# Kernel optimization log

Hardware: AMD Instinct MI355X
Metric: run time of the kernel (lower is better)

## Reference

```python
import jax, jax.numpy as jnp
import numpy as np

BINS = 10


def _neg_pearson(p, t):
    # global standardization (torch.std default is unbiased, ddof=1)
    p = (p - p.mean()) / p.std(ddof=1)
    t = (t - t.mean()) / t.std(ddof=1)
    N = p.shape[1]
    sx = p.sum(1); sy = t.sum(1)
    sxy = (p * t).sum(1)
    sx2 = (p * p).sum(1); sy2 = (t * t).sum(1)
    pear = (N * sxy - sx * sy) / jnp.sqrt((N * sx2 - sx**2) * (N * sy2 - sy**2))
    return (1.0 - pear).mean()


def _hann(N):
    # torch.hann_window is periodic: 0.5*(1 - cos(2*pi*n/N))
    return 0.5 * (1.0 - jnp.cos(2.0 * jnp.pi * jnp.arange(N, dtype=jnp.float32) / N))


def _phase_correlation(x, t):
    # torch.stft with n_fft=seq_len, center=False, hann window -> single frame = rfft(x*hann)
    N = x.shape[1]
    w = _hann(N)
    xf = jnp.fft.rfft(x * w, axis=1)   # [B, N//2+1]
    tf = jnp.fft.rfft(t * w, axis=1)
    corr = xf * jnp.conj(tf)
    corr = corr / jnp.abs(corr)        # phase-only correlation
    cm = jnp.fft.irfft(corr, n=N, axis=1)  # [B, N]
    idx = jnp.argmax(cm, axis=1)
    return 1.0 - jnp.mean(jnp.cos(2.0 * jnp.pi * idx / N))


def _power_spectrum(x, t):
    xp = jnp.abs(jnp.fft.rfft(x, axis=1)) ** 2
    tp = jnp.abs(jnp.fft.rfft(t, axis=1)) ** 2
    return jnp.mean(jnp.abs(xp - tp)) / jnp.mean(tp)


def _mutual_information(x, y, bins=BINS):
    B, S = x.shape
    xmin = x.min(1); xmax = x.max(1)
    ymin = y.min(1); ymax = y.max(1)
    bwx = (xmax - xmin) / bins
    bwy = (ymax - ymin) / bins
    ix = jnp.clip(((x - xmin[:, None]) / bwx[:, None]).astype(jnp.int32), 0, bins - 1)
    iy = jnp.clip(((y - ymin[:, None]) / bwy[:, None]).astype(jnp.int32), 0, bins - 1)
    flat = ix * bins + iy  # [B, S]
    # vectorized 2D histogram via scatter-add (replaces the python double loop)
    hist = jax.vmap(lambda f: jnp.zeros(bins * bins, jnp.float32).at[f].add(1.0))(flat)
    hist = hist.reshape(B, bins, bins)
    hx = hist.sum(2); hy = hist.sum(1)
    denom = B * S  # NOTE: original normalizes by batch*seq (faithful reproduction)
    px = hx / denom; py = hy / denom; pxy = hist / denom
    eps = 1e-8
    mi = (pxy * jnp.log((pxy + eps) / (px[:, :, None] * py[:, None, :] + eps))).sum((1, 2))
    hxe = -(px * jnp.log(px + eps)).sum(1)
    hye = -(py * jnp.log(py + eps)).sum(1)
    nmi = mi / ((hxe + hye) / 2.0)
    return 1.0 - nmi.mean()


def setup_inputs() -> dict:
    key = jax.random.key(0)
    k1, k2 = jax.random.split(key)
    return {
        "predictions": jax.random.normal(k1, (2, 512, 16384), dtype=jnp.float32),
        "targets": jax.random.normal(k2, (512, 16384), dtype=jnp.float32),
        "i": 0,
        "epoch": 700,
    }


def reference(predictions, targets, i, epoch):
    p = predictions[i]  # [B, S]
    loss = _neg_pearson(p, targets)
    if epoch >= 400:
        loss = loss + _phase_correlation(p, targets)
        loss = loss + _power_spectrum(p, targets)
    if epoch >= 700:
        loss = loss + _mutual_information(p, targets)
    return loss
```

## Files before the change

### kernel.cpp

```cpp
#include <hip/hip_runtime.h>
#include <math.h>

#define BB 512
#define SS 16384
#define TPIF 6.28318530717958647692f

#define PAD32(i) ((i) + ((i) >> 5) + ((i) >> 10))
#define NPAD 16912

__device__ __forceinline__ int digrev4(int n) {
    unsigned x = __brev((unsigned)n) >> (32 - 14);
    return (int)(((x & 0x1555u) << 1) | ((x >> 1) & 0x1555u));
}


template <int SGN, int LOG2Q>
__device__ __forceinline__ void stage_dif4(float* sre, float* sim, int t) {
    constexpr int Q = 1 << LOG2Q;
    const float sg = (float)SGN;
    #pragma unroll 2
    for (int c = 0; c < 4; ++c) {
        const int j = 4 * t + c;
        const int g = j >> LOG2Q;
        const int p = j & (Q - 1);
        const int e0 = (g << (LOG2Q + 2)) + p;
        const int i0 = PAD32(e0);
        const int i1 = PAD32(e0 + Q);
        const int i2 = PAD32(e0 + 2 * Q);
        const int i3 = PAD32(e0 + 3 * Q);
        float z0r = sre[i0], z0i = sim[i0];
        float z1r = sre[i1], z1i = sim[i1];
        float z2r = sre[i2], z2i = sim[i2];
        float z3r = sre[i3], z3i = sim[i3];
        float t0r = z0r + z2r, t0i = z0i + z2i;
        float t1r = z0r - z2r, t1i = z0i - z2i;
        float t2r = z1r + z3r, t2i = z1i + z3i;
        float t3r = z1r - z3r, t3i = z1i - z3i;
        float b0r = t0r + t2r, b0i = t0i + t2i;
        float b2r = t0r - t2r, b2i = t0i - t2i;
        float b1r = t1r - sg * t3i, b1i = t1i + sg * t3r;
        float b3r = t1r + sg * t3i, b3i = t1i - sg * t3r;
        const float a = sg * (float)p * (1.0f / (4.0f * (float)Q));
        const float cb = __builtin_amdgcn_cosf(a);
        const float sb = __builtin_amdgcn_sinf(a);
        const float w2r = cb * cb - sb * sb, w2i = 2.0f * cb * sb;
        const float w3r = cb * w2r - sb * w2i, w3i = cb * w2i + sb * w2r;
        sre[i0] = b0r;                    sim[i0] = b0i;
        sre[i1] = b1r * cb - b1i * sb;    sim[i1] = b1r * sb + b1i * cb;
        sre[i2] = b2r * w2r - b2i * w2i;  sim[i2] = b2r * w2i + b2i * w2r;
        sre[i3] = b3r * w3r - b3i * w3i;  sim[i3] = b3r * w3i + b3i * w3r;
    }
    __syncthreads();
}

template <int SGN, int LOG2Q>
__device__ __forceinline__ void stage_dit4(float* sre, float* sim, int t) {
    constexpr int Q = 1 << LOG2Q;
    const float sg = (float)SGN;
    #pragma unroll 2
    for (int c = 0; c < 4; ++c) {
        const int j = 4 * t + c;
        const int g = j >> LOG2Q;
        const int p = j & (Q - 1);
        const int e0 = (g << (LOG2Q + 2)) + p;
        const int i0 = PAD32(e0);
        const int i1 = PAD32(e0 + Q);
        const int i2 = PAD32(e0 + 2 * Q);
        const int i3 = PAD32(e0 + 3 * Q);
        float z0r = sre[i0], z0i = sim[i0];
        float z1r = sre[i1], z1i = sim[i1];
        float z2r = sre[i2], z2i = sim[i2];
        float z3r = sre[i3], z3i = sim[i3];
        const float a = sg * (float)p * (1.0f / (4.0f * (float)Q));
        const float cb = __builtin_amdgcn_cosf(a);
        const float sb = __builtin_amdgcn_sinf(a);
        const float w2r = cb * cb - sb * sb, w2i = 2.0f * cb * sb;
        const float w3r = cb * w2r - sb * w2i, w3i = cb * w2i + sb * w2r;
        float a1r = z1r * cb - z1i * sb,   a1i = z1r * sb + z1i * cb;
        float a2r = z2r * w2r - z2i * w2i, a2i = z2r * w2i + z2i * w2r;
        float a3r = z3r * w3r - z3i * w3i, a3i = z3r * w3i + z3i * w3r;
        float t0r = z0r + a2r, t0i = z0i + a2i;
        float t1r = z0r - a2r, t1i = z0i - a2i;
        float t2r = a1r + a3r, t2i = a1i + a3i;
        float t3r = a1r - a3r, t3i = a1i - a3i;
        sre[i0] = t0r + t2r;       sim[i0] = t0i + t2i;
        sre[i2] = t0r - t2r;       sim[i2] = t0i - t2i;
        sre[i1] = t1r - sg * t3i;  sim[i1] = t1i + sg * t3r;
        sre[i3] = t1r + sg * t3i;  sim[i3] = t1i - sg * t3r;
    }
    __syncthreads();
}

__global__ __launch_bounds__(1024, 4) void k_main(const float* __restrict__ pred,
                                                  const float* __restrict__ targ,
                                                  const int* __restrict__ ip,
                                                  float* __restrict__ wpear,
                                                  float* __restrict__ wcos,
                                                  double* __restrict__ wnum,
                                                  double* __restrict__ wden,
                                                  float* __restrict__ wnmi) {
    __shared__ float sre[NPAD];
    __shared__ float sim[NPAD];
    __shared__ double dpart[16 * 5];
    __shared__ float fpart[16 * 4];
    __shared__ int   subhist[400];
    __shared__ float hxm[10], hym[10];
    __shared__ float mterm[128];
    __shared__ float sbounds[4];
    __shared__ float svalw[16];
    __shared__ int   sidxw[16];

    const int row = blockIdx.x;
    const int t = threadIdx.x;
    const int w = t >> 6;
    const int lane = t & 63;

    const float* xg = pred + (size_t)ip[0] * (size_t)BB * SS + (size_t)row * SS;
    const float* yg = targ + (size_t)row * SS;

    {
        const float4* xg4 = reinterpret_cast<const float4*>(xg);
        const float4* yg4 = reinterpret_cast<const float4*>(yg);
        double sx = 0, sy = 0, sxy = 0, sxx = 0, syy = 0;
        float xmn = 3.4e38f, xmx = -3.4e38f, ymn = 3.4e38f, ymx = -3.4e38f;
        #pragma unroll
        for (int m2 = 0; m2 < 4; ++m2) {
            int idx = t + (m2 << 10);
            float4 a = xg4[idx];
            float4 b = yg4[idx];
            int n0 = idx << 2;
            sre[PAD32(n0 + 0)] = a.x; sim[PAD32(n0 + 0)] = b.x;
            sre[PAD32(n0 + 1)] = a.y; sim[PAD32(n0 + 1)] = b.y;
            sre[PAD32(n0 + 2)] = a.z; sim[PAD32(n0 + 2)] = b.z;
            sre[PAD32(n0 + 3)] = a.w; sim[PAD32(n0 + 3)] = b.w;
            float av[4] = {a.x, a.y, a.z, a.w};
            float bv[4] = {b.x, b.y, b.z, b.w};
            #pragma unroll
            for (int c = 0; c < 4; ++c) {
                float aa = av[c], bb = bv[c];
                sx += (double)aa; sy += (double)bb;
                sxy += (double)aa * (double)bb;
                sxx += (double)aa * (double)aa;
                syy += (double)bb * (double)bb;
                xmn = fminf(xmn, aa); xmx = fmaxf(xmx, aa);
                ymn = fminf(ymn, bb); ymx = fmaxf(ymx, bb);
            }
        }
        #pragma unroll
        for (int o = 32; o > 0; o >>= 1) {
            sx += __shfl_down(sx, o, 64);  sy += __shfl_down(sy, o, 64);
            sxy += __shfl_down(sxy, o, 64);
            sxx += __shfl_down(sxx, o, 64); syy += __shfl_down(syy, o, 64);
            xmn = fminf(xmn, __shfl_down(xmn, o, 64));
            xmx = fmaxf(xmx, __shfl_down(xmx, o, 64));
            ymn = fminf(ymn, __shfl_down(ymn, o, 64));
            ymx = fmaxf(ymx, __shfl_down(ymx, o, 64));
        }
        if (lane == 0) {
            dpart[w*5+0] = sx; dpart[w*5+1] = sy; dpart[w*5+2] = sxy;
            dpart[w*5+3] = sxx; dpart[w*5+4] = syy;
            fpart[w*4+0] = xmn; fpart[w*4+1] = xmx; fpart[w*4+2] = ymn; fpart[w*4+3] = ymx;
        }
    }
    if (t < 400) subhist[t] = 0;
    __syncthreads();
    if (t == 0) {
        double v0=0,v1=0,v2=0,v3=0,v4=0;
        float b0=fpart[0], b1=fpart[1], b2=fpart[2], b3=fpart[3];
        for (int q = 0; q < 16; ++q) {
            v0 += dpart[q*5]; v1 += dpart[q*5+1]; v2 += dpart[q*5+2];
            v3 += dpart[q*5+3]; v4 += dpart[q*5+4];
            b0 = fminf(b0, fpart[q*4]);   b1 = fmaxf(b1, fpart[q*4+1]);
            b2 = fminf(b2, fpart[q*4+2]); b3 = fmaxf(b3, fpart[q*4+3]);
        }
        double N = (double)SS;
        double num = N * v2 - v0 * v1;
        double den = sqrt((N * v3 - v0 * v0) * (N * v4 - v1 * v1));
        wpear[row] = (float)(1.0 - num / den);
        sbounds[0] = b0; sbounds[1] = b1; sbounds[2] = b2; sbounds[3] = b3;
    }
    __syncthreads();

    {
        const float x0 = sbounds[0], bwx = (sbounds[1] - x0) / 10.0f;
        const float y0 = sbounds[2], bwy = (sbounds[3] - y0) / 10.0f;
        int* hsub = subhist + ((t >> 6) & 3) * 100;
        #pragma unroll 2
        for (int m = 0; m < 16; ++m) {
            int ii = PAD32(t + (m << 10));
            float a = sre[ii], b = sim[ii];
            int ix = (int)((a - x0) / bwx); ix = min(max(ix, 0), 9);
            int iy = (int)((b - y0) / bwy); iy = min(max(iy, 0), 9);
            atomicAdd(&hsub[ix * 10 + iy], 1);
        }
    }
    __syncthreads();
    if (t < 100) subhist[t] = subhist[t] + subhist[100+t] + subhist[200+t] + subhist[300+t];
    __syncthreads();
    if (t < 10) {
        int s1 = 0, s2 = 0;
        for (int j = 0; j < 10; ++j) { s1 += subhist[t*10+j]; s2 += subhist[j*10+t]; }
        hxm[t] = (float)s1; hym[t] = (float)s2;
    }
    __syncthreads();
    {
        float term = 0.0f;
        if (t < 100) {
            const float denom = 8388608.0f, eps = 1e-8f;
            float pxy = (float)subhist[t] / denom;
            float px = hxm[t / 10] / denom, py = hym[t % 10] / denom;
            term = pxy * logf((pxy + eps) / (px * py + eps));
        }
        if (t < 128) mterm[t] = (t < 100) ? term : 0.0f;
    }
    __syncthreads();
    if (t == 0) {
        const float denom = 8388608.0f, eps = 1e-8f;
        float mi = 0.0f;
        for (int q = 0; q < 100; ++q) mi += mterm[q];
        float hxe = 0.0f, hye = 0.0f;
        for (int q = 0; q < 10; ++q) {
            float px = hxm[q] / denom, py = hym[q] / denom;
            hxe -= px * logf(px + eps);
            hye -= py * logf(py + eps);
        }
        wnmi[row] = mi / (0.5f * (hxe + hye));
    }
    __syncthreads();

    stage_dif4<-1, 12>(sre, sim, t);
    stage_dif4<-1, 10>(sre, sim, t);
    stage_dif4<-1,  8>(sre, sim, t);
    stage_dif4<-1,  6>(sre, sim, t);
    stage_dif4<-1,  4>(sre, sim, t);
    stage_dif4<-1,  2>(sre, sim, t);
    stage_dif4<-1,  0>(sre, sim, t);

    {
        double anum = 0.0, aden = 0.0;
        float crv[8], civ[8];
        #pragma unroll 1
        for (int m = 0; m < 8; ++m) {
            int k = t + (m << 10);
            int km = (SS - k) & (SS - 1);
            int qa = digrev4(k), qb = digrev4(km);
            float ar  = sre[PAD32(qa)], ai  = sim[PAD32(qa)];
            float cr0 = sre[PAD32(qb)], ci0 = sim[PAD32(qb)];
            float xr = 0.5f * (ar + cr0), xi = 0.5f * (ai - ci0);
            float yr = 0.5f * (ai + ci0), yi = 0.5f * (cr0 - ar);
            float xp = xr * xr + xi * xi;
            float tp = yr * yr + yi * yi;
            anum += (double)fabsf(xp - tp);
            aden += (double)tp;
            int qap = digrev4((k + 1) & (SS - 1));
            int qam = digrev4((k - 1) & (SS - 1));
            int qbp = digrev4((km + 1) & (SS - 1));
            int qbm = digrev4((km - 1) & (SS - 1));
            float apr = sre[PAD32(qap)], api = sim[PAD32(qap)];
            float amr = sre[PAD32(qam)], ami = sim[PAD32(qam)];
            float bpr = sre[PAD32(qbp)], bpi = sim[PAD32(qbp)];
            float bmr = sre[PAD32(qbm)], bmi = sim[PAD32(qbm)];
            float zwr = 0.5f * ar  - 0.25f * (apr + amr);
            float zwi = 0.5f * ai  - 0.25f * (api + ami);
            float vwr = 0.5f * cr0 - 0.25f * (bpr + bmr);
            float vwi = 0.5f * ci0 - 0.25f * (bpi + bmi);
            float xwr = 0.5f * (zwr + vwr), xwi = 0.5f * (zwi - vwi);
            float ywr = 0.5f * (zwi + vwi), ywi = 0.5f * (vwr - zwr);
            float cr = xwr * ywr + xwi * ywi;
            float ci = xwi * ywr - xwr * ywi;
            float mag = sqrtf(cr * cr + ci * ci);
            crv[m] = cr / mag; civ[m] = ci / mag;
        }
        float c8 = 0.0f;
        if (t == 0) {
            int q  = digrev4(8192);
            int qp = digrev4(8193);
            int qm = digrev4(8191);
            float ar = sre[PAD32(q)],  ai = sim[PAD32(q)];
            anum += (double)fabsf(ar * ar - ai * ai);
            aden += (double)(ai * ai);
            float zwr = 0.5f * ar - 0.25f * (sre[PAD32(qp)] + sre[PAD32(qm)]);
            float zwi = 0.5f * ai - 0.25f * (sim[PAD32(qp)] + sim[PAD32(qm)]);
            float pr = zwr * zwi;
            c8 = pr / fabsf(pr);
        }
        #pragma unroll
        for (int o = 32; o > 0; o >>= 1) {
            anum += __shfl_down(anum, o, 64);
            aden += __shfl_down(aden, o, 64);
        }
        if (lane == 0) { dpart[w*2] = anum; dpart[w*2+1] = aden; }
        __syncthreads();
        #pragma unroll
        for (int m = 0; m < 8; ++m) {
            int k = t + (m << 10);
            int km = (SS - k) & (SS - 1);
            int q = digrev4(k), q2 = digrev4(km);
            sre[PAD32(q)]  = crv[m]; sim[PAD32(q)]  = civ[m];
            sre[PAD32(q2)] = crv[m]; sim[PAD32(q2)] = -civ[m];
        }
        if (t == 0) {
            int q = digrev4(8192);
            sre[PAD32(q)] = c8; sim[PAD32(q)] = 0.0f;
            double a = 0, b = 0;
            for (int q2_ = 0; q2_ < 16; ++q2_) { a += dpart[q2_*2]; b += dpart[q2_*2+1]; }
            wnum[row] = a; wden[row] = b;
        }
    }
    __syncthreads();

    stage_dit4<1,  0>(sre, sim, t);
    stage_dit4<1,  2>(sre, sim, t);
    stage_dit4<1,  4>(sre, sim, t);
    stage_dit4<1,  6>(sre, sim, t);
    stage_dit4<1,  8>(sre, sim, t);
    stage_dit4<1, 10>(sre, sim, t);
    stage_dit4<1, 12>(sre, sim, t);

    {
        float bv = -3.4e38f; int bi = 0;
        #pragma unroll
        for (int m = 0; m < 16; ++m) {
            int n = t + (m << 10);
            float v = sre[PAD32(n)];
            if (v > bv) { bv = v; bi = n; }
        }
        #pragma unroll
        for (int o = 32; o > 0; o >>= 1) {
            float v2 = __shfl_down(bv, o, 64);
            int i2 = __shfl_down(bi, o, 64);
            if (v2 > bv || (v2 == bv && i2 < bi)) { bv = v2; bi = i2; }
        }
        if (lane == 0) { svalw[w] = bv; sidxw[w] = bi; }
    }
    __syncthreads();
    if (t == 0) {
        float bv = svalw[0]; int bi = sidxw[0];
        for (int q = 1; q < 16; ++q) {
            if (svalw[q] > bv || (svalw[q] == bv && sidxw[q] < bi)) { bv = svalw[q]; bi = sidxw[q]; }
        }
        wcos[row] = cosf(TPIF * (float)bi / 16384.0f);
    }
}

__global__ __launch_bounds__(512) void k_combine(const float* __restrict__ wpear,
                                                 const float* __restrict__ wcos,
                                                 const double* __restrict__ wnum,
                                                 const double* __restrict__ wden,
                                                 const float* __restrict__ wnmi,
                                                 const int* __restrict__ ep,
                                                 float* __restrict__ out) {
    __shared__ double dp[8 * 5];
    const int tid = threadIdx.x;
    const int w = tid >> 6, lane = tid & 63;
    double v0 = (double)wpear[tid], v1 = (double)wcos[tid];
    double v2 = wnum[tid], v3 = wden[tid], v4 = (double)wnmi[tid];
    #pragma unroll
    for (int o = 32; o > 0; o >>= 1) {
        v0 += __shfl_down(v0, o, 64); v1 += __shfl_down(v1, o, 64);
        v2 += __shfl_down(v2, o, 64); v3 += __shfl_down(v3, o, 64);
        v4 += __shfl_down(v4, o, 64);
    }
    if (lane == 0) {
        dp[w*5+0] = v0; dp[w*5+1] = v1; dp[w*5+2] = v2; dp[w*5+3] = v3; dp[w*5+4] = v4;
    }
    __syncthreads();
    if (tid == 0) {
        double s0=0,s1=0,s2=0,s3=0,s4=0;
        for (int q = 0; q < 8; ++q) {
            s0 += dp[q*5]; s1 += dp[q*5+1]; s2 += dp[q*5+2]; s3 += dp[q*5+3]; s4 += dp[q*5+4];
        }
        int epoch = ep[0];
        double loss = s0 / 512.0;
        if (epoch >= 400) {
            loss += 1.0 - s1 / 512.0;
            loss += s2 / s3;
        }
        if (epoch >= 700) {
            loss += 1.0 - s4 / 512.0;
        }
        out[0] = (float)loss;
    }
}

extern "C" void kernel_launch(void* const* d_in, const int* in_sizes, int n_in,
                              void* d_out, int out_size, void* d_ws, size_t ws_size,
                              hipStream_t stream) {
    const float* pred = (const float*)d_in[0];
    const float* targ = (const float*)d_in[1];
    const int* ip = (const int*)d_in[2];
    const int* ep = (const int*)d_in[3];
    float* out = (float*)d_out;

    double* wnum = (double*)d_ws;
    double* wden = wnum + BB;
    float* wpear = (float*)(wden + BB);
    float* wcos = wpear + BB;
    float* wnmi = wcos + BB;

    k_main<<<dim3(BB), dim3(1024), 0, stream>>>(pred, targ, ip, wpear, wcos, wnum, wden, wnmi);
    k_combine<<<dim3(1), dim3(512), 0, stream>>>(wpear, wcos, wnum, wden, wnmi, ep, out);
}
```

Before: 214.7 us.

## Interleave FFT real/imag in float2 shared array and remap butterfly thread indexing

Replaces the separate real and imaginary shared-memory arrays with one interleaved float2 array, so each complex element is read and written with a single 64-bit LDS access. The padding function changes to suit 8-byte elements. The butterfly-to-thread mapping becomes strided (t + c*1024) instead of contiguous, which changes which LDS addresses a wavefront touches together. The goal is fewer LDS instructions and fewer bank conflicts in the FFT stages. The trade-off is a larger padded footprint (about 140KB of LDS), and some stages may now see different conflict patterns.

Measured after the change: 208.3 us. 3.0% less time.

```diff
diff --git a/kernel.cpp b/kernel.cpp
--- a/kernel.cpp
+++ b/kernel.cpp
@@ -5,8 +5,8 @@
 #define SS 16384
 #define TPIF 6.28318530717958647692f
 
-#define PAD32(i) ((i) + ((i) >> 5) + ((i) >> 10))
-#define NPAD 16912
+#define PD(i) ((i) + ((i) >> 4) + ((i) >> 8))
+#define NPD 17472
 
 __device__ __forceinline__ int digrev4(int n) {
     unsigned x = __brev((unsigned)n) >> (32 - 14);
@@ -15,27 +15,24 @@
 
 
 template <int SGN, int LOG2Q>
-__device__ __forceinline__ void stage_dif4(float* sre, float* sim, int t) {
+__device__ __forceinline__ void stage_dif4(float2* sz, int t) {
     constexpr int Q = 1 << LOG2Q;
     const float sg = (float)SGN;
     #pragma unroll 2
     for (int c = 0; c < 4; ++c) {
-        const int j = 4 * t + c;
+        const int j = t + (c << 10);
         const int g = j >> LOG2Q;
         const int p = j & (Q - 1);
         const int e0 = (g << (LOG2Q + 2)) + p;
-        const int i0 = PAD32(e0);
-        const int i1 = PAD32(e0 + Q);
-        const int i2 = PAD32(e0 + 2 * Q);
-        const int i3 = PAD32(e0 + 3 * Q);
-        float z0r = sre[i0], z0i = sim[i0];
-        float z1r = sre[i1], z1i = sim[i1];
-        float z2r = sre[i2], z2i = sim[i2];
-        float z3r = sre[i3], z3i = sim[i3];
-        float t0r = z0r + z2r, t0i = z0i + z2i;
-        float t1r = z0r - z2r, t1i = z0i - z2i;
-        float t2r = z1r + z3r, t2i = z1i + z3i;
-        float t3r = z1r - z3r, t3i = z1i - z3i;
+        const int i0 = PD(e0);
+        const int i1 = PD(e0 + Q);
+        const int i2 = PD(e0 + 2 * Q);
+        const int i3 = PD(e0 + 3 * Q);
+        float2 z0 = sz[i0], z1 = sz[i1], z2 = sz[i2], z3 = sz[i3];
+        float t0r = z0.x + z2.x, t0i = z0.y + z2.y;
+        float t1r = z0.x - z2.x, t1i = z0.y - z2.y;
+        float t2r = z1.x + z3.x, t2i = z1.y + z3.y;
+        float t3r = z1.x - z3.x, t3i = z1.y - z3.y;
         float b0r = t0r + t2r, b0i = t0i + t2i;
         float b2r = t0r - t2r, b2i = t0i - t2i;
         float b1r = t1r - sg * t3i, b1i = t1i + sg * t3r;
@@ -45,48 +42,45 @@
         const float sb = __builtin_amdgcn_sinf(a);
         const float w2r = cb * cb - sb * sb, w2i = 2.0f * cb * sb;
         const float w3r = cb * w2r - sb * w2i, w3i = cb * w2i + sb * w2r;
-        sre[i0] = b0r;                    sim[i0] = b0i;
-        sre[i1] = b1r * cb - b1i * sb;    sim[i1] = b1r * sb + b1i * cb;
-        sre[i2] = b2r * w2r - b2i * w2i;  sim[i2] = b2r * w2i + b2i * w2r;
-        sre[i3] = b3r * w3r - b3i * w3i;  sim[i3] = b3r * w3i + b3i * w3r;
+        sz[i0] = make_float2(b0r, b0i);
+        sz[i1] = make_float2(b1r * cb - b1i * sb,   b1r * sb + b1i * cb);
+        sz[i2] = make_float2(b2r * w2r - b2i * w2i, b2r * w2i + b2i * w2r);
+        sz[i3] = make_float2(b3r * w3r - b3i * w3i, b3r * w3i + b3i * w3r);
     }
     __syncthreads();
 }
 
 template <int SGN, int LOG2Q>
-__device__ __forceinline__ void stage_dit4(float* sre, float* sim, int t) {
+__device__ __forceinline__ void stage_dit4(float2* sz, int t) {
     constexpr int Q = 1 << LOG2Q;
     const float sg = (float)SGN;
     #pragma unroll 2
     for (int c = 0; c < 4; ++c) {
-        const int j = 4 * t + c;
+        const int j = t + (c << 10);
         const int g = j >> LOG2Q;
         const int p = j & (Q - 1);
         const int e0 = (g << (LOG2Q + 2)) + p;
-        const int i0 = PAD32(e0);
-        const int i1 = PAD32(e0 + Q);
-        const int i2 = PAD32(e0 + 2 * Q);
-        const int i3 = PAD32(e0 + 3 * Q);
-        float z0r = sre[i0], z0i = sim[i0];
-        float z1r = sre[i1], z1i = sim[i1];
-        float z2r = sre[i2], z2i = sim[i2];
-        float z3r = sre[i3], z3i = sim[i3];
+        const int i0 = PD(e0);
+        const int i1 = PD(e0 + Q);
+        const int i2 = PD(e0 + 2 * Q);
+        const int i3 = PD(e0 + 3 * Q);
+        float2 z0 = sz[i0], z1 = sz[i1], z2 = sz[i2], z3 = sz[i3];
         const float a = sg * (float)p * (1.0f / (4.0f * (float)Q));
         const float cb = __builtin_amdgcn_cosf(a);
         const float sb = __builtin_amdgcn_sinf(a);
         const float w2r = cb * cb - sb * sb, w2i = 2.0f * cb * sb;
         const float w3r = cb * w2r - sb * w2i, w3i = cb * w2i + sb * w2r;
-        float a1r = z1r * cb - z1i * sb,   a1i = z1r * sb + z1i * cb;
-        float a2r = z2r * w2r - z2i * w2i, a2i = z2r * w2i + z2i * w2r;
-        float a3r = z3r * w3r - z3i * w3i, a3i = z3r * w3i + z3i * w3r;
-        float t0r = z0r + a2r, t0i = z0i + a2i;
-        float t1r = z0r - a2r, t1i = z0i - a2i;
+        float a1r = z1.x * cb - z1.y * sb,   a1i = z1.x * sb + z1.y * cb;
+        float a2r = z2.x * w2r - z2.y * w2i, a2i = z2.x * w2i + z2.y * w2r;
+        float a3r = z3.x * w3r - z3.y * w3i, a3i = z3.x * w3i + z3.y * w3r;
+        float t0r = z0.x + a2r, t0i = z0.y + a2i;
+        float t1r = z0.x - a2r, t1i = z0.y - a2i;
         float t2r = a1r + a3r, t2i = a1i + a3i;
         float t3r = a1r - a3r, t3i = a1i - a3i;
-        sre[i0] = t0r + t2r;       sim[i0] = t0i + t2i;
-        sre[i2] = t0r - t2r;       sim[i2] = t0i - t2i;
-        sre[i1] = t1r - sg * t3i;  sim[i1] = t1i + sg * t3r;
-        sre[i3] = t1r + sg * t3i;  sim[i3] = t1i - sg * t3r;
+        sz[i0] = make_float2(t0r + t2r, t0i + t2i);
+        sz[i2] = make_float2(t0r - t2r, t0i - t2i);
+        sz[i1] = make_float2(t1r - sg * t3i, t1i + sg * t3r);
+        sz[i3] = make_float2(t1r + sg * t3i, t1i - sg * t3r);
     }
     __syncthreads();
 }
@@ -99,8 +93,7 @@
                                                   double* __restrict__ wnum,
                                                   double* __restrict__ wden,
                                                   float* __restrict__ wnmi) {
-    __shared__ float sre[NPAD];
-    __shared__ float sim[NPAD];
+    __shared__ float2 sz[NPD];
     __shared__ double dpart[16 * 5];
     __shared__ float fpart[16 * 4];
     __shared__ int   subhist[400];
@@ -129,10 +122,10 @@
             float4 a = xg4[idx];
             float4 b = yg4[idx];
             int n0 = idx << 2;
-            sre[PAD32(n0 + 0)] = a.x; sim[PAD32(n0 + 0)] = b.x;
-            sre[PAD32(n0 + 1)] = a.y; sim[PAD32(n0 + 1)] = b.y;
-            sre[PAD32(n0 + 2)] = a.z; sim[PAD32(n0 + 2)] = b.z;
-            sre[PAD32(n0 + 3)] = a.w; sim[PAD32(n0 + 3)] = b.w;
+            sz[PD(n0 + 0)] = make_float2(a.x, b.x);
+            sz[PD(n0 + 1)] = make_float2(a.y, b.y);
+            sz[PD(n0 + 2)] = make_float2(a.z, b.z);
+            sz[PD(n0 + 3)] = make_float2(a.w, b.w);
             float av[4] = {a.x, a.y, a.z, a.w};
             float bv[4] = {b.x, b.y, b.z, b.w};
             #pragma unroll
@@ -187,10 +180,9 @@
         int* hsub = subhist + ((t >> 6) & 3) * 100;
         #pragma unroll 2
         for (int m = 0; m < 16; ++m) {
-            int ii = PAD32(t + (m << 10));
-            float a = sre[ii], b = sim[ii];
-            int ix = (int)((a - x0) / bwx); ix = min(max(ix, 0), 9);
-            int iy = (int)((b - y0) / bwy); iy = min(max(iy, 0), 9);
+            float2 v = sz[PD(t + (m << 10))];
+            int ix = (int)((v.x - x0) / bwx); ix = min(max(ix, 0), 9);
+            int iy = (int)((v.y - y0) / bwy); iy = min(max(iy, 0), 9);
             atomicAdd(&hsub[ix * 10 + iy], 1);
         }
     }
@@ -228,13 +220,13 @@
     }
     __syncthreads();
 
-    stage_dif4<-1, 12>(sre, sim, t);
-    stage_dif4<-1, 10>(sre, sim, t);
-    stage_dif4<-1,  8>(sre, sim, t);
-    stage_dif4<-1,  6>(sre, sim, t);
-    stage_dif4<-1,  4>(sre, sim, t);
-    stage_dif4<-1,  2>(sre, sim, t);
-    stage_dif4<-1,  0>(sre, sim, t);
+    stage_dif4<-1, 12>(sz, t);
+    stage_dif4<-1, 10>(sz, t);
+    stage_dif4<-1,  8>(sz, t);
+    stage_dif4<-1,  6>(sz, t);
+    stage_dif4<-1,  4>(sz, t);
+    stage_dif4<-1,  2>(sz, t);
+    stage_dif4<-1,  0>(sz, t);
 
     {
         double anum = 0.0, aden = 0.0;
@@ -244,26 +236,24 @@
             int k = t + (m << 10);
             int km = (SS - k) & (SS - 1);
             int qa = digrev4(k), qb = digrev4(km);
-            float ar  = sre[PAD32(qa)], ai  = sim[PAD32(qa)];
-            float cr0 = sre[PAD32(qb)], ci0 = sim[PAD32(qb)];
+            float2 za = sz[PD(qa)];
+            float2 zb = sz[PD(qb)];
+            float ar  = za.x, ai  = za.y;
+            float cr0 = zb.x, ci0 = zb.y;
             float xr = 0.5f * (ar + cr0), xi = 0.5f * (ai - ci0);
             float yr = 0.5f * (ai + ci0), yi = 0.5f * (cr0 - ar);
             float xp = xr * xr + xi * xi;
             float tp = yr * yr + yi * yi;
             anum += (double)fabsf(xp - tp);
             aden += (double)tp;
-            int qap = digrev4((k + 1) & (SS - 1));
-            int qam = digrev4((k - 1) & (SS - 1));
-            int qbp = digrev4((km + 1) & (SS - 1));
-            int qbm = digrev4((km - 1) & (SS - 1));
-            float apr = sre[PAD32(qap)], api = sim[PAD32(qap)];
-            float amr = sre[PAD32(qam)], ami = sim[PAD32(qam)];
-            float bpr = sre[PAD32(qbp)], bpi = sim[PAD32(qbp)];
-            float bmr = sre[PAD32(qbm)], bmi = sim[PAD32(qbm)];
-            float zwr = 0.5f * ar  - 0.25f * (apr + amr);
-            float zwi = 0.5f * ai  - 0.25f * (api + ami);
-            float vwr = 0.5f * cr0 - 0.25f * (bpr + bmr);
-            float vwi = 0.5f * ci0 - 0.25f * (bpi + bmi);
+            float2 zap = sz[PD(digrev4((k + 1) & (SS - 1)))];
+            float2 zam = sz[PD(digrev4((k - 1) & (SS - 1)))];
+            float2 zbp = sz[PD(digrev4((km + 1) & (SS - 1)))];
+            float2 zbm = sz[PD(digrev4((km - 1) & (SS - 1)))];
+            float zwr = 0.5f * ar  - 0.25f * (zap.x + zam.x);
+            float zwi = 0.5f * ai  - 0.25f * (zap.y + zam.y);
+            float vwr = 0.5f * cr0 - 0.25f * (zbp.x + zbm.x);
+            float vwi = 0.5f * ci0 - 0.25f * (zbp.y + zbm.y);
             float xwr = 0.5f * (zwr + vwr), xwi = 0.5f * (zwi - vwi);
             float ywr = 0.5f * (zwi + vwi), ywi = 0.5f * (vwr - zwr);
             float cr = xwr * ywr + xwi * ywi;
@@ -273,14 +263,14 @@
         }
         float c8 = 0.0f;
         if (t == 0) {
-            int q  = digrev4(8192);
-            int qp = digrev4(8193);
-            int qm = digrev4(8191);
-            float ar = sre[PAD32(q)],  ai = sim[PAD32(q)];
+            float2 z0 = sz[PD(digrev4(8192))];
+            float2 zp = sz[PD(digrev4(8193))];
+            float2 zm = sz[PD(digrev4(8191))];
+            float ar = z0.x, ai = z0.y;
             anum += (double)fabsf(ar * ar - ai * ai);
             aden += (double)(ai * ai);
-            float zwr = 0.5f * ar - 0.25f * (sre[PAD32(qp)] + sre[PAD32(qm)]);
-            float zwi = 0.5f * ai - 0.25f * (sim[PAD32(qp)] + sim[PAD32(qm)]);
+            float zwr = 0.5f * ar - 0.25f * (zp.x + zm.x);
+            float zwi = 0.5f * ai - 0.25f * (zp.y + zm.y);
             float pr = zwr * zwi;
             c8 = pr / fabsf(pr);
         }
@@ -296,12 +286,11 @@
             int k = t + (m << 10);
             int km = (SS - k) & (SS - 1);
             int q = digrev4(k), q2 = digrev4(km);
-            sre[PAD32(q)]  = crv[m]; sim[PAD32(q)]  = civ[m];
-            sre[PAD32(q2)] = crv[m]; sim[PAD32(q2)] = -civ[m];
+            sz[PD(q)]  = make_float2(crv[m],  civ[m]);
+            sz[PD(q2)] = make_float2(crv[m], -civ[m]);
         }
         if (t == 0) {
-            int q = digrev4(8192);
-            sre[PAD32(q)] = c8; sim[PAD32(q)] = 0.0f;
+            sz[PD(digrev4(8192))] = make_float2(c8, 0.0f);
             double a = 0, b = 0;
             for (int q2_ = 0; q2_ < 16; ++q2_) { a += dpart[q2_*2]; b += dpart[q2_*2+1]; }
             wnum[row] = a; wden[row] = b;
@@ -309,20 +298,20 @@
     }
     __syncthreads();
 
-    stage_dit4<1,  0>(sre, sim, t);
-    stage_dit4<1,  2>(sre, sim, t);
-    stage_dit4<1,  4>(sre, sim, t);
-    stage_dit4<1,  6>(sre, sim, t);
-    stage_dit4<1,  8>(sre, sim, t);
-    stage_dit4<1, 10>(sre, sim, t);
-    stage_dit4<1, 12>(sre, sim, t);
+    stage_dit4<1,  0>(sz, t);
+    stage_dit4<1,  2>(sz, t);
+    stage_dit4<1,  4>(sz, t);
+    stage_dit4<1,  6>(sz, t);
+    stage_dit4<1,  8>(sz, t);
+    stage_dit4<1, 10>(sz, t);
+    stage_dit4<1, 12>(sz, t);
 
     {
         float bv = -3.4e38f; int bi = 0;
         #pragma unroll
         for (int m = 0; m < 16; ++m) {
             int n = t + (m << 10);
-            float v = sre[PAD32(n)];
+            float v = sz[PD(n)].x;
             if (v > bv) { bv = v; bi = n; }
         }
         #pragma unroll
```
